# Optimization experiments

Hardware: AMD Instinct MI355X
Metric: run time of the kernel (lower is better)

Reference implementation:

```python
import jax, jax.numpy as jnp
import numpy as np

N = 50000   # nodes
E = 800000  # edges
IN, H, OUT = 128, 128, 64


def setup_inputs() -> dict:
    key = jax.random.key(0)
    ks = jax.random.split(key, 12)
    x = jax.random.normal(ks[0], (N, IN), dtype=jnp.float32)
    edge_index = jax.random.randint(ks[1], (2, E), 0, N, dtype=jnp.int64)
    edge_weight = jax.random.uniform(ks[2], (E,), dtype=jnp.float32)
    def glorot(k, fi, fo):
        return jax.random.normal(k, (fi, fo), dtype=jnp.float32) * np.float32(1.0 / np.sqrt(fi))
    W1 = glorot(ks[3], IN, H)
    W2 = glorot(ks[4], H, H)
    W3 = glorot(ks[5], H, H)
    W4 = glorot(ks[6], H, OUT)
    b1 = jnp.zeros((H,), jnp.float32)
    b2 = jnp.zeros((H,), jnp.float32)
    b3 = jnp.zeros((H,), jnp.float32)
    b4 = jnp.zeros((OUT,), jnp.float32)
    return dict(x=x, edge_index=edge_index, edge_weight=edge_weight,
                W1=W1, b1=b1, W2=W2, b2=b2, W3=W3, b3=b3, W4=W4, b4=b4)


def _gcn_norm(edge_index, edge_weight, n):
    # PyG gcn_norm: add self-loops (weight 1), symmetric D^{-1/2} A D^{-1/2}.
    loop = jnp.arange(n, dtype=edge_index.dtype)
    src = jnp.concatenate([edge_index[0], loop])
    dst = jnp.concatenate([edge_index[1], loop])
    w = jnp.concatenate([edge_weight, jnp.ones((n,), edge_weight.dtype)])
    deg = jax.ops.segment_sum(w, dst, num_segments=n)
    dinv = jnp.where(deg > 0, jax.lax.rsqrt(deg), 0.0)
    norm = dinv[src] * w * dinv[dst]
    return src, dst, norm


def reference(x, edge_index, edge_weight, W1, b1, W2, b2, W3, b3, W4, b4):
    n = x.shape[0]
    src, dst, norm = _gcn_norm(edge_index, edge_weight, n)  # shared by all layers

    def gcn(h, W, b):
        h = h @ W                                   # [N, F_out]
        msg = h[src] * norm[:, None]                # gather + edge scale
        agg = jax.ops.segment_sum(msg, dst, num_segments=n)  # scatter-add
        return agg + b

    h = jax.nn.relu(gcn(x, W1, b1))   # dropout is identity in eval mode
    h = jax.nn.relu(gcn(h, W2, b2))
    h = jax.nn.relu(gcn(h, W3, b3))
    return jax.nn.sigmoid(gcn(h, W4, b4))
```

## Files before the change

kernel.cpp:

```cpp
#include <hip/hip_runtime.h>
#include <hip/hip_bf16.h>
#include <math.h>


#define FIN 128

typedef __attribute__((ext_vector_type(8))) short bfrag;
typedef __attribute__((ext_vector_type(4))) float f32x4;

__device__ __forceinline__ short f2bf(float f) {
    union { float f; unsigned u; } v; v.f = f;
    unsigned r = v.u + 0x7fff + ((v.u >> 16) & 1);
    return (short)(r >> 16);
}
__device__ __forceinline__ float bflo(unsigned u) {
    union { unsigned x; float f; } c; c.x = u << 16; return c.f;
}
__device__ __forceinline__ float bfhi(unsigned u) {
    union { unsigned x; float f; } c; c.x = u & 0xffff0000u; return c.f;
}
__device__ __forceinline__ float bf1(unsigned short u) {
    union { unsigned x; float f; } c; c.x = (unsigned)u << 16; return c.f;
}


__global__ void prep_wt(const float* __restrict__ W1, const float* __restrict__ W2,
                        const float* __restrict__ W3, const float* __restrict__ W4,
                        short* __restrict__ Wt1, short* __restrict__ Wt2,
                        short* __restrict__ Wt3, short* __restrict__ Wt4,
                        int* __restrict__ cnt, int n) {
    int i = blockIdx.x * 256 + threadIdx.x;
    if (i < n) cnt[i] = 1;
    if (i < 3 * 16384) {
        int m = i >> 14, r = i & 16383;
        const float* W = (m == 0) ? W1 : (m == 1) ? W2 : W3;
        short* Wt = (m == 0) ? Wt1 : (m == 1) ? Wt2 : Wt3;
        int nn = r >> 7, k = r & 127;
        Wt[r] = f2bf(W[k * 128 + nn]);
    } else {
        int r = i - 3 * 16384;
        if (r < 8192) {
            int nn = r >> 7, k = r & 127;
            Wt4[nn * 128 + k] = f2bf(W4[k * 64 + nn]);
        }
    }
}

__global__ void scan_chunk(const int* __restrict__ cnt, int* __restrict__ rowptr,
                           int* __restrict__ bsums, int n) {
    __shared__ int sd[256];
    int t = threadIdx.x;
    int base = blockIdx.x * 1024;
    int v[4]; int local = 0;
#pragma unroll
    for (int j = 0; j < 4; j++) {
        int idx = base + t * 4 + j;
        v[j] = (idx < n) ? cnt[idx] : 0;
        local += v[j];
    }
    sd[t] = local;
    __syncthreads();
    for (int off = 1; off < 256; off <<= 1) {
        int x = (t >= off) ? sd[t - off] : 0;
        __syncthreads();
        sd[t] += x;
        __syncthreads();
    }
    int run = sd[t] - local;
#pragma unroll
    for (int j = 0; j < 4; j++) {
        int idx = base + t * 4 + j;
        run += v[j];
        if (idx < n) rowptr[idx + 1] = run;
    }
    if (t == 255) bsums[blockIdx.x] = sd[255];
}

__global__ void scan_tops(int* bsums, int nchunks, int* rowptr) {
    int l = threadIdx.x;
    if (l == 0) rowptr[0] = 0;
    int v = (l < nchunks) ? bsums[l] : 0;
#pragma unroll
    for (int off = 1; off < 64; off <<= 1) {
        int u = __shfl_up(v, off);
        if (l >= off) v += u;
    }
    if (l < nchunks) bsums[l] = v;
}

__global__ void scan_add(int* rowptr, const int* __restrict__ bsums, int n) {
    int i = blockIdx.x * 256 + threadIdx.x;
    if (i < n) {
        int c = i >> 10;
        if (c > 0) rowptr[i + 1] += bsums[c - 1];
    }
}

__global__ void scatter_csr(const int* __restrict__ src, const int* __restrict__ dst,
                            const float* __restrict__ ew, const unsigned short* __restrict__ posr,
                            const int* __restrict__ rowptr,
                            int* __restrict__ col, float* __restrict__ val, int n, int e) {
    int i = blockIdx.x * 256 + threadIdx.x;
    if (i < n) {
        int p = rowptr[i];
        col[p] = i;
        val[p] = 1.0f;
    } else if (i < n + e) {
        int k = i - n;
        int d = dst[k];
        int p = rowptr[d] + (int)posr[k];
        col[p] = src[k];
        val[p] = ew[k];
    }
}

__global__ void row_dinv(const int* __restrict__ rowptr, const float* __restrict__ val,
                         float* __restrict__ dinv, int n) {
    int i = blockIdx.x * 256 + threadIdx.x;
    if (i < n) {
        int a = rowptr[i], b = rowptr[i + 1];
        float s = 0.f;
        for (int k = a; k < b; k++) s += val[k];
        dinv[i] = rsqrtf(s);
    }
}

__global__ void scale_val(const int* __restrict__ src, const int* __restrict__ dst,
                          const unsigned short* __restrict__ posr, const int* __restrict__ rowptr,
                          const float* __restrict__ dinv, float* __restrict__ val, int n, int e) {
    int i = blockIdx.x * 256 + threadIdx.x;
    if (i < n) {
        val[rowptr[i]] = dinv[i] * dinv[i];
    } else if (i < n + e) {
        int k = i - n;
        int s = src[k], d = dst[k];
        val[rowptr[d] + (int)posr[k]] *= dinv[s] * dinv[d];
    }
}

template<int NOUT, bool AFP32>
__device__ __forceinline__ void mgemm_body(int mblk, const void* Ain,
                                           const short* __restrict__ Wt,
                                           short* __restrict__ out, int nrows) {
    constexpr int NT = NOUT / 16;
    int l = threadIdx.x & 63;
    int lr = l & 15;
    int kg = l >> 4;
    int m0 = mblk * 64 + (threadIdx.x >> 6) * 16;
    int arow = m0 + lr;
    bool rowok = arow < nrows;

    bfrag a[4];
    if (AFP32) {
        const float* A = (const float*)Ain + (size_t)arow * 128 + kg * 8;
#pragma unroll
        for (int kc = 0; kc < 4; kc++) {
            bfrag t;
            if (rowok) {
                float4 u0 = *(const float4*)(A + kc * 32);
                float4 u1 = *(const float4*)(A + kc * 32 + 4);
                t[0] = f2bf(u0.x); t[1] = f2bf(u0.y); t[2] = f2bf(u0.z); t[3] = f2bf(u0.w);
                t[4] = f2bf(u1.x); t[5] = f2bf(u1.y); t[6] = f2bf(u1.z); t[7] = f2bf(u1.w);
            } else {
#pragma unroll
                for (int j = 0; j < 8; j++) t[j] = 0;
            }
            a[kc] = t;
        }
    } else {
        const short* A = (const short*)Ain + (size_t)arow * 128 + kg * 8;
#pragma unroll
        for (int kc = 0; kc < 4; kc++) {
            if (rowok) {
                a[kc] = *(const bfrag*)(A + kc * 32);
            } else {
#pragma unroll
                for (int j = 0; j < 8; j++) a[kc][j] = 0;
            }
        }
    }

    f32x4 acc[NT];
#pragma unroll
    for (int t = 0; t < NT; t++)
#pragma unroll
        for (int j = 0; j < 4; j++) acc[t][j] = 0.f;

#pragma unroll
    for (int nt = 0; nt < NT; nt++) {
        const short* Wc = Wt + (size_t)(nt * 16 + lr) * 128 + kg * 8;
#pragma unroll
        for (int kc = 0; kc < 4; kc++) {
            bfrag b = *(const bfrag*)(Wc + kc * 32);
            acc[nt] = __builtin_amdgcn_mfma_f32_16x16x32_bf16(a[kc], b, acc[nt], 0, 0, 0);
        }
    }

#pragma unroll
    for (int nt = 0; nt < NT; nt++) {
#pragma unroll
        for (int r = 0; r < 4; r++) {
            int orow = m0 + kg * 4 + r;
            if (orow >= nrows) continue;
            int ocol = nt * 16 + lr;
            out[(size_t)orow * NOUT + ocol] = f2bf(acc[nt][r]);
        }
    }
}

template<int NOUT, bool AFP32>
__global__ __launch_bounds__(256) void mgemm_kernel(const void* __restrict__ Ain,
                                                    const short* __restrict__ Wt,
                                                    short* __restrict__ out, int nrows) {
    mgemm_body<NOUT, AFP32>(blockIdx.x, Ain, Wt, out, nrows);
}

__global__ __launch_bounds__(256) void fused_hist_gemm1(const int* __restrict__ dst,
                                                        int* __restrict__ cnt,
                                                        unsigned short* __restrict__ posr, int e,
                                                        const float* __restrict__ x,
                                                        const short* __restrict__ Wt1,
                                                        short* __restrict__ B, int nrows) {
    const int stride = gridDim.x * 256;
    int i = blockIdx.x * 256 + threadIdx.x;
    for (; i + 3 * stride < e; i += 4 * stride) {
        int d0 = dst[i];
        int d1 = dst[i + stride];
        int d2 = dst[i + 2 * stride];
        int d3 = dst[i + 3 * stride];
        int p0 = atomicAdd(&cnt[d0], 1);
        int p1 = atomicAdd(&cnt[d1], 1);
        int p2 = atomicAdd(&cnt[d2], 1);
        int p3 = atomicAdd(&cnt[d3], 1);
        posr[i]              = (unsigned short)p0;
        posr[i + stride]     = (unsigned short)p1;
        posr[i + 2 * stride] = (unsigned short)p2;
        posr[i + 3 * stride] = (unsigned short)p3;
    }
    for (; i < e; i += stride) posr[i] = (unsigned short)atomicAdd(&cnt[dst[i]], 1);

    mgemm_body<128, true>(blockIdx.x, x, Wt1, B, nrows);
}

template<int F, int EPI, int OB>
__global__ __launch_bounds__(256) void agg_kernel(const unsigned short* __restrict__ h,
                                                  const int* __restrict__ rowptr,
                                                  const int* __restrict__ col,
                                                  const float* __restrict__ val,
                                                  const float* __restrict__ bias,
                                                  void* __restrict__ outv, int n) {
    int wv = threadIdx.x >> 6;
    int lane = threadIdx.x & 63;
    int row = blockIdx.x * 4 + wv;
    if (row >= n) return;
    int e0 = rowptr[row], e1 = rowptr[row + 1];

    if (F == 128) {
        const unsigned short* hb = h + 2 * lane;
        float2 a0 = {0.f, 0.f}, a1 = {0.f, 0.f}, a2 = {0.f, 0.f}, a3 = {0.f, 0.f};
        float2 a4 = {0.f, 0.f}, a5 = {0.f, 0.f}, a6 = {0.f, 0.f}, a7 = {0.f, 0.f};
        int e = e0;
        for (; e + 8 <= e1; e += 8) {
            int s0 = col[e+0], s1 = col[e+1], s2 = col[e+2], s3 = col[e+3];
            int s4 = col[e+4], s5 = col[e+5], s6 = col[e+6], s7 = col[e+7];
            float v0 = val[e+0], v1 = val[e+1], v2 = val[e+2], v3 = val[e+3];
            float v4 = val[e+4], v5 = val[e+5], v6 = val[e+6], v7 = val[e+7];
            unsigned u0 = *(const unsigned*)&hb[(size_t)s0 * 128];
            unsigned u1 = *(const unsigned*)&hb[(size_t)s1 * 128];
            unsigned u2 = *(const unsigned*)&hb[(size_t)s2 * 128];
            unsigned u3 = *(const unsigned*)&hb[(size_t)s3 * 128];
            unsigned u4 = *(const unsigned*)&hb[(size_t)s4 * 128];
            unsigned u5 = *(const unsigned*)&hb[(size_t)s5 * 128];
            unsigned u6 = *(const unsigned*)&hb[(size_t)s6 * 128];
            unsigned u7 = *(const unsigned*)&hb[(size_t)s7 * 128];
            a0.x = fmaf(v0, bflo(u0), a0.x); a0.y = fmaf(v0, bfhi(u0), a0.y);
            a1.x = fmaf(v1, bflo(u1), a1.x); a1.y = fmaf(v1, bfhi(u1), a1.y);
            a2.x = fmaf(v2, bflo(u2), a2.x); a2.y = fmaf(v2, bfhi(u2), a2.y);
            a3.x = fmaf(v3, bflo(u3), a3.x); a3.y = fmaf(v3, bfhi(u3), a3.y);
            a4.x = fmaf(v4, bflo(u4), a4.x); a4.y = fmaf(v4, bfhi(u4), a4.y);
            a5.x = fmaf(v5, bflo(u5), a5.x); a5.y = fmaf(v5, bfhi(u5), a5.y);
            a6.x = fmaf(v6, bflo(u6), a6.x); a6.y = fmaf(v6, bfhi(u6), a6.y);
            a7.x = fmaf(v7, bflo(u7), a7.x); a7.y = fmaf(v7, bfhi(u7), a7.y);
        }
        if (e + 4 <= e1) {
            int s0 = col[e+0], s1 = col[e+1], s2 = col[e+2], s3 = col[e+3];
            float v0 = val[e+0], v1 = val[e+1], v2 = val[e+2], v3 = val[e+3];
            unsigned u0 = *(const unsigned*)&hb[(size_t)s0 * 128];
            unsigned u1 = *(const unsigned*)&hb[(size_t)s1 * 128];
            unsigned u2 = *(const unsigned*)&hb[(size_t)s2 * 128];
            unsigned u3 = *(const unsigned*)&hb[(size_t)s3 * 128];
            a0.x = fmaf(v0, bflo(u0), a0.x); a0.y = fmaf(v0, bfhi(u0), a0.y);
            a1.x = fmaf(v1, bflo(u1), a1.x); a1.y = fmaf(v1, bfhi(u1), a1.y);
            a2.x = fmaf(v2, bflo(u2), a2.x); a2.y = fmaf(v2, bfhi(u2), a2.y);
            a3.x = fmaf(v3, bflo(u3), a3.x); a3.y = fmaf(v3, bfhi(u3), a3.y);
            e += 4;
        }
        for (; e < e1; ++e) {
            float v = val[e];
            unsigned u = *(const unsigned*)&hb[(size_t)col[e] * 128];
            a0.x = fmaf(v, bflo(u), a0.x); a0.y = fmaf(v, bfhi(u), a0.y);
        }
        float2 r;
        r.x = ((a0.x + a1.x) + (a2.x + a3.x)) + ((a4.x + a5.x) + (a6.x + a7.x));
        r.y = ((a0.y + a1.y) + (a2.y + a3.y)) + ((a4.y + a5.y) + (a6.y + a7.y));
        if (EPI == 1) {
            r.x = fmaxf(r.x + bias[2 * lane + 0], 0.f);
            r.y = fmaxf(r.y + bias[2 * lane + 1], 0.f);
        }
        if (OB == 1) {
            unsigned pk = (unsigned)(unsigned short)f2bf(r.x)
                        | ((unsigned)(unsigned short)f2bf(r.y) << 16);
            ((unsigned*)outv)[(size_t)row * 64 + lane] = pk;
        } else {
            *(float2*)&((float*)outv)[(size_t)row * 128 + 2 * lane] = r;
        }
    } else {
        const unsigned short* hb = h + lane;
        float a0 = 0.f, a1 = 0.f, a2 = 0.f, a3 = 0.f;
        float a4 = 0.f, a5 = 0.f, a6 = 0.f, a7 = 0.f;
        int e = e0;
        for (; e + 8 <= e1; e += 8) {
            int s0 = col[e+0], s1 = col[e+1], s2 = col[e+2], s3 = col[e+3];
            int s4 = col[e+4], s5 = col[e+5], s6 = col[e+6], s7 = col[e+7];
            float v0 = val[e+0], v1 = val[e+1], v2 = val[e+2], v3 = val[e+3];
            float v4 = val[e+4], v5 = val[e+5], v6 = val[e+6], v7 = val[e+7];
            float g0 = bf1(hb[(size_t)s0 * 64]);
            float g1 = bf1(hb[(size_t)s1 * 64]);
            float g2 = bf1(hb[(size_t)s2 * 64]);
            float g3 = bf1(hb[(size_t)s3 * 64]);
            float g4 = bf1(hb[(size_t)s4 * 64]);
            float g5 = bf1(hb[(size_t)s5 * 64]);
            float g6 = bf1(hb[(size_t)s6 * 64]);
            float g7 = bf1(hb[(size_t)s7 * 64]);
            a0 = fmaf(v0, g0, a0); a1 = fmaf(v1, g1, a1);
            a2 = fmaf(v2, g2, a2); a3 = fmaf(v3, g3, a3);
            a4 = fmaf(v4, g4, a4); a5 = fmaf(v5, g5, a5);
            a6 = fmaf(v6, g6, a6); a7 = fmaf(v7, g7, a7);
        }
        if (e + 4 <= e1) {
            int s0 = col[e+0], s1 = col[e+1], s2 = col[e+2], s3 = col[e+3];
            float v0 = val[e+0], v1 = val[e+1], v2 = val[e+2], v3 = val[e+3];
            a0 = fmaf(v0, bf1(hb[(size_t)s0 * 64]), a0);
            a1 = fmaf(v1, bf1(hb[(size_t)s1 * 64]), a1);
            a2 = fmaf(v2, bf1(hb[(size_t)s2 * 64]), a2);
            a3 = fmaf(v3, bf1(hb[(size_t)s3 * 64]), a3);
            e += 4;
        }
        for (; e < e1; ++e) a0 = fmaf(val[e], bf1(hb[(size_t)col[e] * 64]), a0);
        float acc = ((a0 + a1) + (a2 + a3)) + ((a4 + a5) + (a6 + a7));
        if (EPI == 2) {
            acc += bias[lane];
            acc = 1.0f / (1.0f + __expf(-acc));
        }
        ((float*)outv)[(size_t)row * 64 + lane] = acc;
    }
}


extern "C" void kernel_launch(void* const* d_in, const int* in_sizes, int n_in,
                              void* d_out, int out_size, void* d_ws, size_t ws_size,
                              hipStream_t stream) {
    const float* x  = (const float*)d_in[0];
    const int*   ei = (const int*)d_in[1];
    const float* ew = (const float*)d_in[2];
    const float* W1 = (const float*)d_in[3];
    const float* b1 = (const float*)d_in[4];
    const float* W2 = (const float*)d_in[5];
    const float* b2 = (const float*)d_in[6];
    const float* W3 = (const float*)d_in[7];
    const float* b3 = (const float*)d_in[8];
    const float* W4 = (const float*)d_in[9];
    const float* b4 = (const float*)d_in[10];

    const int N = in_sizes[0] / FIN;
    const int E = in_sizes[1] / 2;
    const int M = N + E;
    const int* srcI = ei;
    const int* dstI = ei + E;

    char* p = (char*)d_ws;
    auto alloc = [&](size_t bytes) -> void* {
        void* r = (void*)p;
        p += (bytes + 255) & ~(size_t)255;
        return r;
    };
    float* dinv   = (float*)alloc((size_t)N * 4);
    int*   cnt    = (int*)  alloc((size_t)N * 4);
    int*   rowptr = (int*)  alloc((size_t)(N + 1) * 4);
    unsigned short* posr = (unsigned short*)alloc((size_t)E * 2);
    int*   col    = (int*)  alloc((size_t)M * 4);
    float* val    = (float*)alloc((size_t)M * 4);
    int*   bsums  = (int*)  alloc(256 * 4);
    short* B      = (short*)alloc((size_t)N * 128 * 2);
    short* G      = (short*)alloc((size_t)N * 128 * 2);
    short* Wt1    = (short*)alloc(16384 * 2);
    short* Wt2    = (short*)alloc(16384 * 2);
    short* Wt3    = (short*)alloc(16384 * 2);
    short* Wt4    = (short*)alloc(8192 * 2);

    int gN = (N + 255) / 256;
    int gG = (N + 63) / 64;
    int gA = (N + 3) / 4;
    int gM = (N + E + 255) / 256;
    int nchunks = (N + 1023) / 1024;

    prep_wt<<<224, 256, 0, stream>>>(W1, W2, W3, W4, Wt1, Wt2, Wt3, Wt4, cnt, N);
    fused_hist_gemm1<<<gG, 256, 0, stream>>>(dstI, cnt, posr, E, x, Wt1, B, N);
    scan_chunk<<<nchunks, 256, 0, stream>>>(cnt, rowptr, bsums, N);
    scan_tops<<<1, 64, 0, stream>>>(bsums, nchunks, rowptr);
    scan_add<<<gN, 256, 0, stream>>>(rowptr, bsums, N);
    scatter_csr<<<gM, 256, 0, stream>>>(srcI, dstI, ew, posr, rowptr, col, val, N, E);
    row_dinv<<<gN, 256, 0, stream>>>(rowptr, val, dinv, N);
    scale_val<<<gM, 256, 0, stream>>>(srcI, dstI, posr, rowptr, dinv, val, N, E);

    agg_kernel<128, 1, 1><<<gA, 256, 0, stream>>>((const unsigned short*)B, rowptr, col, val, b1, G, N);
    mgemm_kernel<128, false><<<gG, 256, 0, stream>>>(G, Wt2, B, N);
    agg_kernel<128, 1, 1><<<gA, 256, 0, stream>>>((const unsigned short*)B, rowptr, col, val, b2, G, N);
    mgemm_kernel<128, false><<<gG, 256, 0, stream>>>(G, Wt3, B, N);
    agg_kernel<128, 1, 1><<<gA, 256, 0, stream>>>((const unsigned short*)B, rowptr, col, val, b3, G, N);
    mgemm_kernel<64, false><<<gG, 256, 0, stream>>>(G, Wt4, B, N);
    agg_kernel<64, 2, 0><<<gA, 256, 0, stream>>>((const unsigned short*)B, rowptr, col, val, b4, d_out, N);
}
```

Before: 408.0 us.

## Fuse aggregation with next-layer GEMM and merge scan and scale kernels

Each hidden layer's aggregation (bias+ReLU) now writes its 16-row tile to shared memory and immediately runs the next layer's MFMA GEMM, removing the intermediate activation round trip and three separate GEMM launches. The histogram is split onto dedicated blocks instead of being done before the GEMM in every block. The scan_tops kernel is folded into scan_add, and edge normalization switches from a per-edge pass using posr to a per-row CSR pass. The fused kernel uses 16-row blocks with 4 rows per wave, which may reduce latency hiding for the gather, and the per-row scale loop runs serially over each row's edges.

```diff
diff --git a/kernel.cpp b/kernel.cpp
--- a/kernel.cpp
+++ b/kernel.cpp
@@ -4,6 +4,7 @@
 
 
 #define FIN 128
+#define HIST_BLOCKS 256
 
 typedef __attribute__((ext_vector_type(8))) short bfrag;
 typedef __attribute__((ext_vector_type(4))) float f32x4;
@@ -76,23 +77,24 @@
     if (t == 255) bsums[blockIdx.x] = sd[255];
 }
 
-__global__ void scan_tops(int* bsums, int nchunks, int* rowptr) {
-    int l = threadIdx.x;
-    if (l == 0) rowptr[0] = 0;
-    int v = (l < nchunks) ? bsums[l] : 0;
-#pragma unroll
-    for (int off = 1; off < 64; off <<= 1) {
-        int u = __shfl_up(v, off);
-        if (l >= off) v += u;
-    }
-    if (l < nchunks) bsums[l] = v;
-}
-
-__global__ void scan_add(int* rowptr, const int* __restrict__ bsums, int n) {
+__global__ void scan_add(int* rowptr, const int* __restrict__ bsums, int n, int nchunks) {
+    __shared__ int pref[64];
+    if (threadIdx.x < 64) {
+        int l = threadIdx.x;
+        int v = (l < nchunks) ? bsums[l] : 0;
+#pragma unroll
+        for (int off = 1; off < 64; off <<= 1) {
+            int u = __shfl_up(v, off);
+            if (l >= off) v += u;
+        }
+        pref[l] = v;
+    }
+    __syncthreads();
     int i = blockIdx.x * 256 + threadIdx.x;
+    if (i == 0) rowptr[0] = 0;
     if (i < n) {
         int c = i >> 10;
-        if (c > 0) rowptr[i + 1] += bsums[c - 1];
+        if (c > 0) rowptr[i + 1] += pref[c - 1];
     }
 }
 
@@ -125,16 +127,13 @@
     }
 }
 
-__global__ void scale_val(const int* __restrict__ src, const int* __restrict__ dst,
-                          const unsigned short* __restrict__ posr, const int* __restrict__ rowptr,
-                          const float* __restrict__ dinv, float* __restrict__ val, int n, int e) {
+__global__ void scale_row(const int* __restrict__ rowptr, const int* __restrict__ col,
+                          const float* __restrict__ dinv, float* __restrict__ val, int n) {
     int i = blockIdx.x * 256 + threadIdx.x;
     if (i < n) {
-        val[rowptr[i]] = dinv[i] * dinv[i];
-    } else if (i < n + e) {
-        int k = i - n;
-        int s = src[k], d = dst[k];
-        val[rowptr[d] + (int)posr[k]] *= dinv[s] * dinv[d];
+        int a = rowptr[i], b = rowptr[i + 1];
+        float di = dinv[i];
+        for (int k = a; k < b; k++) val[k] *= di * dinv[col[k]];
     }
 }
 
@@ -208,152 +207,200 @@
     }
 }
 
-template<int NOUT, bool AFP32>
-__global__ __launch_bounds__(256) void mgemm_kernel(const void* __restrict__ Ain,
-                                                    const short* __restrict__ Wt,
-                                                    short* __restrict__ out, int nrows) {
-    mgemm_body<NOUT, AFP32>(blockIdx.x, Ain, Wt, out, nrows);
-}
-
 __global__ __launch_bounds__(256) void fused_hist_gemm1(const int* __restrict__ dst,
                                                         int* __restrict__ cnt,
                                                         unsigned short* __restrict__ posr, int e,
                                                         const float* __restrict__ x,
                                                         const short* __restrict__ Wt1,
                                                         short* __restrict__ B, int nrows) {
-    const int stride = gridDim.x * 256;
-    int i = blockIdx.x * 256 + threadIdx.x;
-    for (; i + 3 * stride < e; i += 4 * stride) {
-        int d0 = dst[i];
-        int d1 = dst[i + stride];
-        int d2 = dst[i + 2 * stride];
-        int d3 = dst[i + 3 * stride];
-        int p0 = atomicAdd(&cnt[d0], 1);
-        int p1 = atomicAdd(&cnt[d1], 1);
-        int p2 = atomicAdd(&cnt[d2], 1);
-        int p3 = atomicAdd(&cnt[d3], 1);
-        posr[i]              = (unsigned short)p0;
-        posr[i + stride]     = (unsigned short)p1;
-        posr[i + 2 * stride] = (unsigned short)p2;
-        posr[i + 3 * stride] = (unsigned short)p3;
-    }
-    for (; i < e; i += stride) posr[i] = (unsigned short)atomicAdd(&cnt[dst[i]], 1);
-
-    mgemm_body<128, true>(blockIdx.x, x, Wt1, B, nrows);
-}
-
-template<int F, int EPI, int OB>
-__global__ __launch_bounds__(256) void agg_kernel(const unsigned short* __restrict__ h,
-                                                  const int* __restrict__ rowptr,
-                                                  const int* __restrict__ col,
-                                                  const float* __restrict__ val,
-                                                  const float* __restrict__ bias,
-                                                  void* __restrict__ outv, int n) {
+    if (blockIdx.x < HIST_BLOCKS) {
+        const int stride = HIST_BLOCKS * 256;
+        int i = blockIdx.x * 256 + threadIdx.x;
+        for (; i + 3 * stride < e; i += 4 * stride) {
+            int d0 = dst[i];
+            int d1 = dst[i + stride];
+            int d2 = dst[i + 2 * stride];
+            int d3 = dst[i + 3 * stride];
+            int p0 = atomicAdd(&cnt[d0], 1);
+            int p1 = atomicAdd(&cnt[d1], 1);
+            int p2 = atomicAdd(&cnt[d2], 1);
+            int p3 = atomicAdd(&cnt[d3], 1);
+            posr[i]              = (unsigned short)p0;
+            posr[i + stride]     = (unsigned short)p1;
+            posr[i + 2 * stride] = (unsigned short)p2;
+            posr[i + 3 * stride] = (unsigned short)p3;
+        }
+        for (; i < e; i += stride) posr[i] = (unsigned short)atomicAdd(&cnt[dst[i]], 1);
+        return;
+    }
+    mgemm_body<128, true>(blockIdx.x - HIST_BLOCKS, x, Wt1, B, nrows);
+}
+
+__device__ __forceinline__ float2 agg_row128(const unsigned short* __restrict__ h,
+                                             const int* __restrict__ col,
+                                             const float* __restrict__ val,
+                                             int e0, int e1, int lane) {
+    const unsigned short* hb = h + 2 * lane;
+    float2 a0 = {0.f, 0.f}, a1 = {0.f, 0.f}, a2 = {0.f, 0.f}, a3 = {0.f, 0.f};
+    float2 a4 = {0.f, 0.f}, a5 = {0.f, 0.f}, a6 = {0.f, 0.f}, a7 = {0.f, 0.f};
+    int e = e0;
+    for (; e + 8 <= e1; e += 8) {
+        int s0 = col[e+0], s1 = col[e+1], s2 = col[e+2], s3 = col[e+3];
+        int s4 = col[e+4], s5 = col[e+5], s6 = col[e+6], s7 = col[e+7];
+        float v0 = val[e+0], v1 = val[e+1], v2 = val[e+2], v3 = val[e+3];
+        float v4 = val[e+4], v5 = val[e+5], v6 = val[e+6], v7 = val[e+7];
+        unsigned u0 = *(const unsigned*)&hb[(size_t)s0 * 128];
+        unsigned u1 = *(const unsigned*)&hb[(size_t)s1 * 128];
+        unsigned u2 = *(const unsigned*)&hb[(size_t)s2 * 128];
+        unsigned u3 = *(const unsigned*)&hb[(size_t)s3 * 128];
+        unsigned u4 = *(const unsigned*)&hb[(size_t)s4 * 128];
+        unsigned u5 = *(const unsigned*)&hb[(size_t)s5 * 128];
+        unsigned u6 = *(const unsigned*)&hb[(size_t)s6 * 128];
+        unsigned u7 = *(const unsigned*)&hb[(size_t)s7 * 128];
+        a0.x = fmaf(v0, bflo(u0), a0.x); a0.y = fmaf(v0, bfhi(u0), a0.y);
+        a1.x = fmaf(v1, bflo(u1), a1.x); a1.y = fmaf(v1, bfhi(u1), a1.y);
+        a2.x = fmaf(v2, bflo(u2), a2.x); a2.y = fmaf(v2, bfhi(u2), a2.y);
+        a3.x = fmaf(v3, bflo(u3), a3.x); a3.y = fmaf(v3, bfhi(u3), a3.y);
+        a4.x = fmaf(v4, bflo(u4), a4.x); a4.y = fmaf(v4, bfhi(u4), a4.y);
+        a5.x = fmaf(v5, bflo(u5), a5.x); a5.y = fmaf(v5, bfhi(u5), a5.y);
+        a6.x = fmaf(v6, bflo(u6), a6.x); a6.y = fmaf(v6, bfhi(u6), a6.y);
+        a7.x = fmaf(v7, bflo(u7), a7.x); a7.y = fmaf(v7, bfhi(u7), a7.y);
+    }
+    if (e + 4 <= e1) {
+        int s0 = col[e+0], s1 = col[e+1], s2 = col[e+2], s3 = col[e+3];
+        float v0 = val[e+0], v1 = val[e+1], v2 = val[e+2], v3 = val[e+3];
+        unsigned u0 = *(const unsigned*)&hb[(size_t)s0 * 128];
+        unsigned u1 = *(const unsigned*)&hb[(size_t)s1 * 128];
+        unsigned u2 = *(const unsigned*)&hb[(size_t)s2 * 128];
+        unsigned u3 = *(const unsigned*)&hb[(size_t)s3 * 128];
+        a0.x = fmaf(v0, bflo(u0), a0.x); a0.y = fmaf(v0, bfhi(u0), a0.y);
+        a1.x = fmaf(v1, bflo(u1), a1.x); a1.y = fmaf(v1, bfhi(u1), a1.y);
+        a2.x = fmaf(v2, bflo(u2), a2.x); a2.y = fmaf(v2, bfhi(u2), a2.y);
+        a3.x = fmaf(v3, bflo(u3), a3.x); a3.y = fmaf(v3, bfhi(u3), a3.y);
+        e += 4;
+    }
+    for (; e < e1; ++e) {
+        float v = val[e];
+        unsigned u = *(const unsigned*)&hb[(size_t)col[e] * 128];
+        a0.x = fmaf(v, bflo(u), a0.x); a0.y = fmaf(v, bfhi(u), a0.y);
+    }
+    float2 r;
+    r.x = ((a0.x + a1.x) + (a2.x + a3.x)) + ((a4.x + a5.x) + (a6.x + a7.x));
+    r.y = ((a0.y + a1.y) + (a2.y + a3.y)) + ((a4.y + a5.y) + (a6.y + a7.y));
+    return r;
+}
+
+template<int NOUT>
+__global__ __launch_bounds__(256) void agg_gemm_kernel(const unsigned short* __restrict__ h,
+                                                       const int* __restrict__ rowptr,
+                                                       const int* __restrict__ col,
+                                                       const float* __restrict__ val,
+                                                       const float* __restrict__ bias,
+                                                       const short* __restrict__ Wt,
+                                                       short* __restrict__ out, int n) {
+    __shared__ short As[16][136];
+    int wv = threadIdx.x >> 6;
+    int lane = threadIdx.x & 63;
+    int r0 = blockIdx.x * 16;
+
+#pragma unroll
+    for (int rr = 0; rr < 4; rr++) {
+        int row = r0 + wv * 4 + rr;
+        float2 r = {0.f, 0.f};
+        if (row < n) {
+            int e0 = rowptr[row], e1 = rowptr[row + 1];
+            r = agg_row128(h, col, val, e0, e1, lane);
+            r.x = fmaxf(r.x + bias[2 * lane + 0], 0.f);
+            r.y = fmaxf(r.y + bias[2 * lane + 1], 0.f);
+        }
+        unsigned pk = (unsigned)(unsigned short)f2bf(r.x)
+                    | ((unsigned)(unsigned short)f2bf(r.y) << 16);
+        ((unsigned*)&As[wv * 4 + rr][0])[lane] = pk;
+    }
+    __syncthreads();
+
+    constexpr int NT = NOUT / 64;
+    int lr = lane & 15, kg = lane >> 4;
+    bfrag a[4];
+#pragma unroll
+    for (int kc = 0; kc < 4; kc++)
+        a[kc] = *(const bfrag*)&As[lr][kg * 8 + kc * 32];
+
+    f32x4 acc[NT];
+#pragma unroll
+    for (int t = 0; t < NT; t++)
+#pragma unroll
+        for (int j = 0; j < 4; j++) acc[t][j] = 0.f;
+
+#pragma unroll
+    for (int nt = 0; nt < NT; nt++) {
+        int ocol = wv * (NOUT / 4) + nt * 16 + lr;
+        const short* Wc = Wt + (size_t)ocol * 128 + kg * 8;
+#pragma unroll
+        for (int kc = 0; kc < 4; kc++) {
+            bfrag b = *(const bfrag*)(Wc + kc * 32);
+            acc[nt] = __builtin_amdgcn_mfma_f32_16x16x32_bf16(a[kc], b, acc[nt], 0, 0, 0);
+        }
+    }
+
+#pragma unroll
+    for (int nt = 0; nt < NT; nt++) {
+        int ocol = wv * (NOUT / 4) + nt * 16 + lr;
+#pragma unroll
+        for (int r = 0; r < 4; r++) {
+            int orow = r0 + kg * 4 + r;
+            if (orow < n) out[(size_t)orow * NOUT + ocol] = f2bf(acc[nt][r]);
+        }
+    }
+}
+
+__global__ __launch_bounds__(256) void agg64_kernel(const unsigned short* __restrict__ h,
+                                                    const int* __restrict__ rowptr,
+                                                    const int* __restrict__ col,
+                                                    const float* __restrict__ val,
+                                                    const float* __restrict__ bias,
+                                                    float* __restrict__ out, int n) {
     int wv = threadIdx.x >> 6;
     int lane = threadIdx.x & 63;
     int row = blockIdx.x * 4 + wv;
     if (row >= n) return;
     int e0 = rowptr[row], e1 = rowptr[row + 1];
-
-    if (F == 128) {
-        const unsigned short* hb = h + 2 * lane;
-        float2 a0 = {0.f, 0.f}, a1 = {0.f, 0.f}, a2 = {0.f, 0.f}, a3 = {0.f, 0.f};
-        float2 a4 = {0.f, 0.f}, a5 = {0.f, 0.f}, a6 = {0.f, 0.f}, a7 = {0.f, 0.f};
-        int e = e0;
-        for (; e + 8 <= e1; e += 8) {
-            int s0 = col[e+0], s1 = col[e+1], s2 = col[e+2], s3 = col[e+3];
-            int s4 = col[e+4], s5 = col[e+5], s6 = col[e+6], s7 = col[e+7];
-            float v0 = val[e+0], v1 = val[e+1], v2 = val[e+2], v3 = val[e+3];
-            float v4 = val[e+4], v5 = val[e+5], v6 = val[e+6], v7 = val[e+7];
-            unsigned u0 = *(const unsigned*)&hb[(size_t)s0 * 128];
-            unsigned u1 = *(const unsigned*)&hb[(size_t)s1 * 128];
-            unsigned u2 = *(const unsigned*)&hb[(size_t)s2 * 128];
-            unsigned u3 = *(const unsigned*)&hb[(size_t)s3 * 128];
-            unsigned u4 = *(const unsigned*)&hb[(size_t)s4 * 128];
-            unsigned u5 = *(const unsigned*)&hb[(size_t)s5 * 128];
-            unsigned u6 = *(const unsigned*)&hb[(size_t)s6 * 128];
-            unsigned u7 = *(const unsigned*)&hb[(size_t)s7 * 128];
-            a0.x = fmaf(v0, bflo(u0), a0.x); a0.y = fmaf(v0, bfhi(u0), a0.y);
-            a1.x = fmaf(v1, bflo(u1), a1.x); a1.y = fmaf(v1, bfhi(u1), a1.y);
-            a2.x = fmaf(v2, bflo(u2), a2.x); a2.y = fmaf(v2, bfhi(u2), a2.y);
-            a3.x = fmaf(v3, bflo(u3), a3.x); a3.y = fmaf(v3, bfhi(u3), a3.y);
-            a4.x = fmaf(v4, bflo(u4), a4.x); a4.y = fmaf(v4, bfhi(u4), a4.y);
-            a5.x = fmaf(v5, bflo(u5), a5.x); a5.y = fmaf(v5, bfhi(u5), a5.y);
-            a6.x = fmaf(v6, bflo(u6), a6.x); a6.y = fmaf(v6, bfhi(u6), a6.y);
-            a7.x = fmaf(v7, bflo(u7), a7.x); a7.y = fmaf(v7, bfhi(u7), a7.y);
-        }
-        if (e + 4 <= e1) {
-            int s0 = col[e+0], s1 = col[e+1], s2 = col[e+2], s3 = col[e+3];
-            float v0 = val[e+0], v1 = val[e+1], v2 = val[e+2], v3 = val[e+3];
-            unsigned u0 = *(const unsigned*)&hb[(size_t)s0 * 128];
-            unsigned u1 = *(const unsigned*)&hb[(size_t)s1 * 128];
-            unsigned u2 = *(const unsigned*)&hb[(size_t)s2 * 128];
-            unsigned u3 = *(const unsigned*)&hb[(size_t)s3 * 128];
-            a0.x = fmaf(v0, bflo(u0), a0.x); a0.y = fmaf(v0, bfhi(u0), a0.y);
-            a1.x = fmaf(v1, bflo(u1), a1.x); a1.y = fmaf(v1, bfhi(u1), a1.y);
-            a2.x = fmaf(v2, bflo(u2), a2.x); a2.y = fmaf(v2, bfhi(u2), a2.y);
-            a3.x = fmaf(v3, bflo(u3), a3.x); a3.y = fmaf(v3, bfhi(u3), a3.y);
-            e += 4;
-        }
-        for (; e < e1; ++e) {
-            float v = val[e];
-            unsigned u = *(const unsigned*)&hb[(size_t)col[e] * 128];
-            a0.x = fmaf(v, bflo(u), a0.x); a0.y = fmaf(v, bfhi(u), a0.y);
-        }
-        float2 r;
-        r.x = ((a0.x + a1.x) + (a2.x + a3.x)) + ((a4.x + a5.x) + (a6.x + a7.x));
-        r.y = ((a0.y + a1.y) + (a2.y + a3.y)) + ((a4.y + a5.y) + (a6.y + a7.y));
-        if (EPI == 1) {
-            r.x = fmaxf(r.x + bias[2 * lane + 0], 0.f);
-            r.y = fmaxf(r.y + bias[2 * lane + 1], 0.f);
-        }
-        if (OB == 1) {
-            unsigned pk = (unsigned)(unsigned short)f2bf(r.x)
-                        | ((unsigned)(unsigned short)f2bf(r.y) << 16);
-            ((unsigned*)outv)[(size_t)row * 64 + lane] = pk;
-        } else {
-            *(float2*)&((float*)outv)[(size_t)row * 128 + 2 * lane] = r;
-        }
-    } else {
-        const unsigned short* hb = h + lane;
-        float a0 = 0.f, a1 = 0.f, a2 = 0.f, a3 = 0.f;
-        float a4 = 0.f, a5 = 0.f, a6 = 0.f, a7 = 0.f;
-        int e = e0;
-        for (; e + 8 <= e1; e += 8) {
-            int s0 = col[e+0], s1 = col[e+1], s2 = col[e+2], s3 = col[e+3];
-            int s4 = col[e+4], s5 = col[e+5], s6 = col[e+6], s7 = col[e+7];
-            float v0 = val[e+0], v1 = val[e+1], v2 = val[e+2], v3 = val[e+3];
-            float v4 = val[e+4], v5 = val[e+5], v6 = val[e+6], v7 = val[e+7];
-            float g0 = bf1(hb[(size_t)s0 * 64]);
-            float g1 = bf1(hb[(size_t)s1 * 64]);
-            float g2 = bf1(hb[(size_t)s2 * 64]);
-            float g3 = bf1(hb[(size_t)s3 * 64]);
-            float g4 = bf1(hb[(size_t)s4 * 64]);
-            float g5 = bf1(hb[(size_t)s5 * 64]);
-            float g6 = bf1(hb[(size_t)s6 * 64]);
-            float g7 = bf1(hb[(size_t)s7 * 64]);
-            a0 = fmaf(v0, g0, a0); a1 = fmaf(v1, g1, a1);
-            a2 = fmaf(v2, g2, a2); a3 = fmaf(v3, g3, a3);
-            a4 = fmaf(v4, g4, a4); a5 = fmaf(v5, g5, a5);
-            a6 = fmaf(v6, g6, a6); a7 = fmaf(v7, g7, a7);
-        }
-        if (e + 4 <= e1) {
-            int s0 = col[e+0], s1 = col[e+1], s2 = col[e+2], s3 = col[e+3];
-            float v0 = val[e+0], v1 = val[e+1], v2 = val[e+2], v3 = val[e+3];
-            a0 = fmaf(v0, bf1(hb[(size_t)s0 * 64]), a0);
-            a1 = fmaf(v1, bf1(hb[(size_t)s1 * 64]), a1);
-            a2 = fmaf(v2, bf1(hb[(size_t)s2 * 64]), a2);
-            a3 = fmaf(v3, bf1(hb[(size_t)s3 * 64]), a3);
-            e += 4;
-        }
-        for (; e < e1; ++e) a0 = fmaf(val[e], bf1(hb[(size_t)col[e] * 64]), a0);
-        float acc = ((a0 + a1) + (a2 + a3)) + ((a4 + a5) + (a6 + a7));
-        if (EPI == 2) {
-            acc += bias[lane];
-            acc = 1.0f / (1.0f + __expf(-acc));
-        }
-        ((float*)outv)[(size_t)row * 64 + lane] = acc;
-    }
+    const unsigned short* hb = h + lane;
+    float a0 = 0.f, a1 = 0.f, a2 = 0.f, a3 = 0.f;
+    float a4 = 0.f, a5 = 0.f, a6 = 0.f, a7 = 0.f;
+    int e = e0;
+    for (; e + 8 <= e1; e += 8) {
+        int s0 = col[e+0], s1 = col[e+1], s2 = col[e+2], s3 = col[e+3];
+        int s4 = col[e+4], s5 = col[e+5], s6 = col[e+6], s7 = col[e+7];
+        float v0 = val[e+0], v1 = val[e+1], v2 = val[e+2], v3 = val[e+3];
+        float v4 = val[e+4], v5 = val[e+5], v6 = val[e+6], v7 = val[e+7];
+        float g0 = bf1(hb[(size_t)s0 * 64]);
+        float g1 = bf1(hb[(size_t)s1 * 64]);
+        float g2 = bf1(hb[(size_t)s2 * 64]);
+        float g3 = bf1(hb[(size_t)s3 * 64]);
+        float g4 = bf1(hb[(size_t)s4 * 64]);
+        float g5 = bf1(hb[(size_t)s5 * 64]);
+        float g6 = bf1(hb[(size_t)s6 * 64]);
+        float g7 = bf1(hb[(size_t)s7 * 64]);
+        a0 = fmaf(v0, g0, a0); a1 = fmaf(v1, g1, a1);
+        a2 = fmaf(v2, g2, a2); a3 = fmaf(v3, g3, a3);
+        a4 = fmaf(v4, g4, a4); a5 = fmaf(v5, g5, a5);
+        a6 = fmaf(v6, g6, a6); a7 = fmaf(v7, g7, a7);
+    }
+    if (e + 4 <= e1) {
+        int s0 = col[e+0], s1 = col[e+1], s2 = col[e+2], s3 = col[e+3];
+        float v0 = val[e+0], v1 = val[e+1], v2 = val[e+2], v3 = val[e+3];
+        a0 = fmaf(v0, bf1(hb[(size_t)s0 * 64]), a0);
+        a1 = fmaf(v1, bf1(hb[(size_t)s1 * 64]), a1);
+        a2 = fmaf(v2, bf1(hb[(size_t)s2 * 64]), a2);
+        a3 = fmaf(v3, bf1(hb[(size_t)s3 * 64]), a3);
+        e += 4;
+    }
+    for (; e < e1; ++e) a0 = fmaf(val[e], bf1(hb[(size_t)col[e] * 64]), a0);
+    float acc = ((a0 + a1) + (a2 + a3)) + ((a4 + a5) + (a6 + a7));
+    acc += bias[lane];
+    acc = 1.0f / (1.0f + __expf(-acc));
+    out[(size_t)row * 64 + lane] = acc;
 }
 
 
@@ -391,33 +438,31 @@
     int*   col    = (int*)  alloc((size_t)M * 4);
     float* val    = (float*)alloc((size_t)M * 4);
     int*   bsums  = (int*)  alloc(256 * 4);
-    short* B      = (short*)alloc((size_t)N * 128 * 2);
-    short* G      = (short*)alloc((size_t)N * 128 * 2);
+    short* Ba     = (short*)alloc((size_t)N * 128 * 2);
+    short* Bb     = (short*)alloc((size_t)N * 128 * 2);
     short* Wt1    = (short*)alloc(16384 * 2);
     short* Wt2    = (short*)alloc(16384 * 2);
     short* Wt3    = (short*)alloc(16384 * 2);
     short* Wt4    = (short*)alloc(8192 * 2);
 
-    int gN = (N + 255) / 256;
-    int gG = (N + 63) / 64;
-    int gA = (N + 3) / 4;
-    int gM = (N + E + 255) / 256;
+    int gN  = (N + 255) / 256;
+    int gG  = (N + 63) / 64;
+    int gAG = (N + 15) / 16;
+    int gA4 = (N + 3) / 4;
+    int gM  = (N + E + 255) / 256;
     int nchunks = (N + 1023) / 1024;
 
     prep_wt<<<224, 256, 0, stream>>>(W1, W2, W3, W4, Wt1, Wt2, Wt3, Wt4, cnt, N);
-    fused_hist_gemm1<<<gG, 256, 0, stream>>>(dstI, cnt, posr, E, x, Wt1, B, N);
+    fused_hist_gemm1<<<HIST_BLOCKS + gG, 256, 0, stream>>>(dstI, cnt, posr, E,
+                                                           x, Wt1, Ba, N);
     scan_chunk<<<nchunks, 256, 0, stream>>>(cnt, rowptr, bsums, N);
-    scan_tops<<<1, 64, 0, stream>>>(bsums, nchunks, rowptr);
-    scan_add<<<gN, 256, 0, stream>>>(rowptr, bsums, N);
+    scan_add<<<gN, 256, 0, stream>>>(rowptr, bsums, N, nchunks);
     scatter_csr<<<gM, 256, 0, stream>>>(srcI, dstI, ew, posr, rowptr, col, val, N, E);
     row_dinv<<<gN, 256, 0, stream>>>(rowptr, val, dinv, N);
-    scale_val<<<gM, 256, 0, stream>>>(srcI, dstI, posr, rowptr, dinv, val, N, E);
-
-    agg_kernel<128, 1, 1><<<gA, 256, 0, stream>>>((const unsigned short*)B, rowptr, col, val, b1, G, N);
-    mgemm_kernel<128, false><<<gG, 256, 0, stream>>>(G, Wt2, B, N);
-    agg_kernel<128, 1, 1><<<gA, 256, 0, stream>>>((const unsigned short*)B, rowptr, col, val, b2, G, N);
-    mgemm_kernel<128, false><<<gG, 256, 0, stream>>>(G, Wt3, B, N);
-    agg_kernel<128, 1, 1><<<gA, 256, 0, stream>>>((const unsigned short*)B, rowptr, col, val, b3, G, N);
-    mgemm_kernel<64, false><<<gG, 256, 0, stream>>>(G, Wt4, B, N);
-    agg_kernel<64, 2, 0><<<gA, 256, 0, stream>>>((const unsigned short*)B, rowptr, col, val, b4, d_out, N);
-}
+    scale_row<<<gN, 256, 0, stream>>>(rowptr, col, dinv, val, N);
+
+    agg_gemm_kernel<128><<<gAG, 256, 0, stream>>>((const unsigned short*)Ba, rowptr, col, val, b1, Wt2, Bb, N);
+    agg_gemm_kernel<128><<<gAG, 256, 0, stream>>>((const unsigned short*)Bb, rowptr, col, val, b2, Wt3, Ba, N);
+    agg_gemm_kernel<64><<<gAG, 256, 0, stream>>>((const unsigned short*)Ba, rowptr, col, val, b3, Wt4, Bb, N);
+    agg64_kernel<<<gA4, 256, 0, stream>>>((const unsigned short*)Bb, rowptr, col, val, b4, (float*)d_out, N);
+}
```

After: 365.5 us. -10.4%, faster.
